# Kernel tuning notes

Measured on AMD Instinct MI355X. Metric: run time of the kernel, lower is better.

The kernel has to match this reference:

```python
import jax, jax.numpy as jnp
import numpy as np

DEPTH = 2
DIM = 512
FF = 2048
INNER = 32
VOCAB = 8192
B = 2
L = 512
LN_EPS = 1e-5


def _layer_norm(x, g, b):
    m = jnp.mean(x, axis=-1, keepdims=True)
    v = jnp.var(x, axis=-1, keepdims=True)
    return (x - m) * jax.lax.rsqrt(v + LN_EPS) * g + b


def _sioconv_layer(x, wa, wx, v_re, v_im, h0_re, h0_im, w_ol):
    # x: [B, L, DIM] float32
    Bb, Ll, _ = x.shape
    I = v_re.shape[0]
    # complex gate a with magnitude sigmoid(log|a|^2)
    af = (x @ wa.T).reshape(Bb, Ll, I, 2)
    a = jax.lax.complex(af[..., 0], af[..., 1])
    m = jnp.square(af[..., 0]) + jnp.square(af[..., 1])
    a = a * jax.lax.rsqrt(m) * jax.nn.sigmoid(jnp.log(m))  # [B,L,I] complex
    # complex input x with magnitude |x| (x * rsqrt(|x|^2) * |x|^2)
    xf = (x @ wx.T).reshape(Bb, Ll, I, 2)
    xc = jax.lax.complex(xf[..., 0], xf[..., 1])
    mx = jnp.square(xf[..., 0]) + jnp.square(xf[..., 1])
    xc = xc * jax.lax.rsqrt(mx) * mx  # [B,L,I] complex
    # cumulative log-decay products: the original's FFT conv of the upper-
    # triangular a_ln against an all-ones matrix is exactly a cumsum along j.
    a_ln = jnp.log(a)  # [B,L,I]
    ii = jnp.arange(Ll)[:, None]
    jj = jnp.arange(Ll)[None, :]
    tri = jnp.where((jj >= ii)[None, None, :, :],
                    jnp.transpose(a_ln, (0, 2, 1))[:, :, None, :],
                    jnp.zeros((), a_ln.dtype))  # [B,I,L,L]: tri[b,d,i,j]=a_ln[b,j,d] for j>=i
    s = jnp.cumsum(tri, axis=3)
    # c[b,d,i,j] = prod_{t=i..j} a[b,t,d] for j>=i; =1 at j=i-1; 0 below.
    c = jnp.where((jj >= ii - 1)[None, None, :, :], jnp.exp(s), jnp.zeros((), s.dtype))
    V = jax.lax.complex(v_re, v_im)
    Vinv = jnp.linalg.inv(V)
    h0 = jax.lax.complex(h0_re, h0_im)  # [I]
    xct = jnp.transpose(xc, (0, 2, 1))  # [B,I,L]
    x_roll = jnp.roll(xct, 1, axis=2).at[:, :, 0].set(h0[None, :])
    # original builds C[b,l,m,n,o] = V diag(c) V^-1 then einsum; contract lazily:
    y = jnp.einsum('ko,bol->bkl', Vinv, x_roll)  # eigenbasis inputs [B,I,L]
    t = jnp.einsum('bkij,bki->bjk', c, y)        # recurrence in eigenbasis [B,L,I]
    h = jnp.einsum('bjk,nk->bjn', t, V)          # back to state basis [B,L,I]
    h = h.at[:, -1, :].add(xc[:, -1, :])         # last step input (others already in c via j=i-1 band)
    return jnp.real(h) @ w_ol.T


def setup_inputs() -> dict:
    key = jax.random.key(0)
    ks = jax.random.split(key, 16)
    f = lambda k, shp: jax.random.normal(k, shp, dtype=jnp.float32)
    return {
        'x': f(ks[0], (B, L, VOCAB)),
        'w_in': f(ks[1], (DIM, VOCAB)) * VOCAB ** -0.5,
        'b_in': jnp.zeros((DIM,), jnp.float32),
        'ln1_g': jnp.ones((DEPTH, DIM), jnp.float32),
        'ln1_b': jnp.zeros((DEPTH, DIM), jnp.float32),
        'wa': f(ks[2], (DEPTH, 2 * INNER, DIM)) * DIM ** -0.5,
        'wx': f(ks[3], (DEPTH, 2 * INNER, DIM)) * DIM ** -0.5,
        'v_re': f(ks[4], (DEPTH, INNER, INNER)),
        'v_im': f(ks[5], (DEPTH, INNER, INNER)),
        'h0_re': f(ks[6], (DEPTH, INNER)),
        'h0_im': f(ks[7], (DEPTH, INNER)),
        'w_ol': f(ks[8], (DEPTH, DIM, INNER)) * INNER ** -0.5,
        'ln2_g': jnp.ones((DEPTH, DIM), jnp.float32),
        'ln2_b': jnp.zeros((DEPTH, DIM), jnp.float32),
        'w1': f(ks[9], (DEPTH, FF, DIM)) * DIM ** -0.5,
        'b1': jnp.zeros((DEPTH, FF), jnp.float32),
        'w2': f(ks[10], (DEPTH, DIM, FF)) * FF ** -0.5,
        'b2': jnp.zeros((DEPTH, DIM), jnp.float32),
        'lnl_g': jnp.ones((DIM,), jnp.float32),
        'lnl_b': jnp.zeros((DIM,), jnp.float32),
        'w_out': f(ks[11], (VOCAB, DIM)) * DIM ** -0.5,
        'b_out': jnp.zeros((VOCAB,), jnp.float32),
    }


def reference(x, w_in, b_in, ln1_g, ln1_b, wa, wx, v_re, v_im, h0_re, h0_im,
              w_ol, ln2_g, ln2_b, w1, b1, w2, b2, lnl_g, lnl_b, w_out, b_out):
    h = x @ w_in.T + b_in  # [B,L,DIM]
    for d in range(DEPTH):
        r = h
        z = _layer_norm(h, ln1_g[d], ln1_b[d])
        z = _sioconv_layer(z, wa[d], wx[d], v_re[d], v_im[d], h0_re[d], h0_im[d], w_ol[d])
        h = z + r
        r = h
        z = _layer_norm(h, ln2_g[d], ln2_b[d])
        z = jax.nn.silu(z @ w1[d].T + b1[d]) @ w2[d].T + b2[d]
        h = z + r
    h = _layer_norm(h, lnl_g, lnl_b)
    return h @ w_out.T + b_out
```

## Files before the change

### kernel.cpp

```cpp
#include <hip/hip_runtime.h>
#include <stdint.h>

#define DEPTHC 2
#define DIMC   512
#define FFC    2048
#define INNERC 32
#define VOCABC 8192
#define BC     2
#define LC     512
#define NTOK   1024

typedef _Float16 f16;
typedef __attribute__((ext_vector_type(8))) _Float16 f16x8;
typedef __attribute__((ext_vector_type(4))) float f32x4;

__device__ __forceinline__ float2 cmul2(float2 a, float2 b){
    return make_float2(a.x*b.x - a.y*b.y, a.x*b.y + a.y*b.x);
}
__device__ __forceinline__ float2 cadd2(float2 a, float2 b){
    return make_float2(a.x + b.x, a.y + b.y);
}

__device__ __forceinline__ void gl_lds16(const void* g, void* l){
    __builtin_amdgcn_global_load_lds(
        (const __attribute__((address_space(1))) unsigned int*)g,
        (__attribute__((address_space(3))) unsigned int*)l, 16, 0, 0);
}

__device__ __forceinline__ void cvt16(const float* s, f16* d){
    float4 v0 = ((const float4*)s)[0], v1 = ((const float4*)s)[1];
    float4 v2 = ((const float4*)s)[2], v3 = ((const float4*)s)[3];
    union { f16 h[16]; float4 f4[2]; } u;
    u.h[0]=(f16)v0.x; u.h[1]=(f16)v0.y; u.h[2]=(f16)v0.z; u.h[3]=(f16)v0.w;
    u.h[4]=(f16)v1.x; u.h[5]=(f16)v1.y; u.h[6]=(f16)v1.z; u.h[7]=(f16)v1.w;
    u.h[8]=(f16)v2.x; u.h[9]=(f16)v2.y; u.h[10]=(f16)v2.z; u.h[11]=(f16)v2.w;
    u.h[12]=(f16)v3.x; u.h[13]=(f16)v3.y; u.h[14]=(f16)v3.z; u.h[15]=(f16)v3.w;
    ((float4*)d)[0] = u.f4[0]; ((float4*)d)[1] = u.f4[1];
}

__global__ __launch_bounds__(256) void k_prep(
    const float* __restrict__ s1, const float* __restrict__ s2,
    const float* __restrict__ s3, const float* __restrict__ s4,
    const float* __restrict__ wa4, const float* __restrict__ wx4,
    f16* __restrict__ d1, f16* __restrict__ d2,
    f16* __restrict__ d3, f16* __restrict__ d4, f16* __restrict__ wgb,
    int n1, int n2, int n3, int n4,
    const float* __restrict__ v_re, const float* __restrict__ v_im,
    const float* __restrict__ h0re, const float* __restrict__ h0im,
    float2* __restrict__ vinv, float2* __restrict__ h0c)
{
    __shared__ float2 M[32][64];
    if (blockIdx.x < 2){
        const int d = blockIdx.x;
        const int tid = threadIdx.x;
        const int c = tid & 63;
        const int wv = tid >> 6;
        if (tid < 32) h0c[d*32 + tid] = make_float2(h0re[d*32 + tid], h0im[d*32 + tid]);
#pragma unroll
        for (int rr = 0; rr < 8; ++rr){
            int r = wv*8 + rr;
            float re, im;
            if (c < 32){ re = v_re[d*1024 + r*32 + c]; im = v_im[d*1024 + r*32 + c]; }
            else       { re = (c - 32 == r) ? 1.f : 0.f; im = 0.f; }
            M[r][c] = make_float2(re, im);
        }
        __syncthreads();
#pragma unroll 1
        for (int col = 0; col < 32; ++col){
            float2 prow = M[col][c];
            float pvx = __shfl(prow.x, col, 64);
            float pvy = __shfl(prow.y, col, 64);
            float dm = pvx*pvx + pvy*pvy;
            float ir = pvx/dm, ii = -pvy/dm;
            float2 nv = make_float2(prow.x*ir - prow.y*ii, prow.x*ii + prow.y*ir);
#pragma unroll
            for (int rr = 0; rr < 8; ++rr){
                int r = wv*8 + rr;
                if (r == col) continue;
                float2 f  = M[r][col];
                float2 m0 = M[r][c];
                m0.x -= f.x*nv.x - f.y*nv.y;
                m0.y -= f.x*nv.y + f.y*nv.x;
                M[r][c] = m0;
            }
            __syncthreads();
        }
        if (c >= 32){
#pragma unroll
            for (int rr = 0; rr < 8; ++rr){
                int r = wv*8 + rr;
                float2 dv = M[r][r];
                float dm = dv.x*dv.x + dv.y*dv.y;
                float ir = dv.x/dm, ii = -dv.y/dm;
                float2 m0 = M[r][c];
                vinv[d*1024 + r*32 + (c - 32)] =
                    make_float2(m0.x*ir - m0.y*ii, m0.x*ii + m0.y*ir);
            }
        }
        return;
    }
    long long i = ((long long)(blockIdx.x - 2) * 256 + threadIdx.x) * 16;
    const float* s; f16* d;
    if (i < n1){ s = s1; d = d1; }
    else { i -= n1;
        if (i < n2){ s = s2; d = d2; }
        else { i -= n2;
            if (i < n3){ s = s3; d = d3; }
            else { i -= n3;
                if (i < n4){ s = s4; d = d4; }
                else {
                    i -= n4;
                    if (i >= 131072) return;
                    const float* gs; f16* gd;
                    if (i < 65536){
                        int dd = (int)(i >> 15), rem = (int)(i & 32767);
                        gs = wa4 + i; gd = wgb + dd*65536 + rem;
                    } else {
                        long long e2 = i - 65536;
                        int dd = (int)(e2 >> 15), rem = (int)(e2 & 32767);
                        gs = wx4 + e2; gd = wgb + dd*65536 + 32768 + rem;
                    }
                    cvt16(gs, gd);
                    return;
                }
            }
        }
    }
    cvt16(s + i, d + i);
}

template<int MT, int NT, int MODE, int ASRC>
__global__ __launch_bounds__(256) void k_gemmT(
    const void* __restrict__ Av, const f16* __restrict__ Bw,
    void* __restrict__ C, const float* __restrict__ bias,
    int N, int K, int klen, int partStride,
    float2* __restrict__ a_tp, float2* __restrict__ xcp)
{
    constexpr int RM = MT/32, RN = NT/32;
    __shared__ __align__(16) f16 As[MT*64];
    __shared__ __align__(16) f16 Bs[NT*64];
    const int tid = threadIdx.x;
    const int m0 = blockIdx.y * MT;
    const int n0 = blockIdx.x * NT;
    const int kbeg = blockIdx.z * klen;
    const int l = tid & 63;
    const int w = tid >> 6;
    const int fr = l & 15;
    const int fq = l >> 4;
    const int kx = l & 7;
    const int wm = (w >> 1) * (MT/2);
    const int wn = (w & 1) * (NT/2);
    const int srow = tid >> 3;
    const int schunk = (tid & 7) ^ (srow & 7);
    const f16*   gA16 = (const f16*)Av + (ASRC ? 0 : ((size_t)(m0 + srow) * K + kbeg + schunk * 8));
    const float* gA32 = (const float*)Av + (ASRC ? ((size_t)(m0 + srow) * K + kbeg + (tid & 7) * 8) : 0);
    const f16* gB = Bw + (size_t)(n0 + srow) * K + kbeg + schunk * 8;
    const size_t rowskip = (size_t)32 * K;
    f16* lA = As + tid * 8;
    f16* lAw = As + srow * 64 + schunk * 8;
    f16* lB = Bs + tid * 8;
    f32x4 acc[RM][RN];
#pragma unroll
    for (int i = 0; i < RM; ++i)
#pragma unroll
        for (int j = 0; j < RN; ++j)
            acc[i][j] = (f32x4){0.f, 0.f, 0.f, 0.f};
    for (int kk = 0; kk < klen; kk += 64){
        __syncthreads();
        if (ASRC){
#pragma unroll
            for (int i = 0; i < MT/32; ++i){
                float4 va = *(const float4*)(gA32 + i*rowskip);
                float4 vb = *(const float4*)(gA32 + i*rowskip + 4);
                union { f16 h[8]; f16x8 v; } u;
                u.h[0]=(f16)va.x; u.h[1]=(f16)va.y; u.h[2]=(f16)va.z; u.h[3]=(f16)va.w;
                u.h[4]=(f16)vb.x; u.h[5]=(f16)vb.y; u.h[6]=(f16)vb.z; u.h[7]=(f16)vb.w;
                *(f16x8*)(lAw + i*2048) = u.v;
            }
            gA32 += 64;
        } else {
#pragma unroll
            for (int i = 0; i < MT/32; ++i) gl_lds16(gA16 + i*rowskip, lA + i*2048);
            gA16 += 64;
        }
#pragma unroll
        for (int i = 0; i < NT/32; ++i) gl_lds16(gB + i*rowskip, lB + i*2048);
        gB += 64;
        __syncthreads();
#pragma unroll
        for (int h = 0; h < 2; ++h){
            f16x8 af[RM], bf[RN];
#pragma unroll
            for (int i = 0; i < RM; ++i)
                af[i] = *(const f16x8*)(As + (wm + 16*i + fr) * 64 + (((h*4 + fq) ^ kx)) * 8);
#pragma unroll
            for (int j = 0; j < RN; ++j)
                bf[j] = *(const f16x8*)(Bs + (wn + 16*j + fr) * 64 + (((h*4 + fq) ^ kx)) * 8);
#pragma unroll
            for (int i = 0; i < RM; ++i)
#pragma unroll
                for (int j = 0; j < RN; ++j)
                    acc[i][j] = __builtin_amdgcn_mfma_f32_16x16x32_f16(af[i], bf[j], acc[i][j], 0, 0, 0);
        }
    }
#pragma unroll
    for (int i = 0; i < RM; ++i)
#pragma unroll
        for (int j = 0; j < RN; ++j)
#pragma unroll
            for (int r = 0; r < 4; ++r){
                int row = m0 + wm + 16*i + fq*4 + r;
                int col = n0 + wn + 16*j + fr;
                if (MODE == 1){
                    ((f16*)C + (size_t)blockIdx.z * partStride)[(size_t)row * N + col] = (f16)acc[i][j][r];
                } else if (MODE == 0){
                    ((float*)C)[(size_t)row * N + col] = acc[i][j][r] + bias[col];
                } else if (MODE == 2){
                    float v = acc[i][j][r] + bias[col];
                    ((f16*)C)[(size_t)row * N + col] = (f16)(v / (1.f + __expf(-v)));
                } else {
                    float val = acc[i][j][r];
                    float pv = __shfl_xor(val, 1, 64);
                    if (!(fr & 1)){
                        float re = val, im = pv;
                        int bb = row >> 9, t = row & 511;
                        float m2 = re*re + im*im;
                        if (col < 64){
                            int k = col >> 1;
                            float sa = rsqrtf(m2) * (m2 / (1.f + m2));
                            a_tp[(size_t)(bb*INNERC + k)*LC + t] = make_float2(re*sa, im*sa);
                        } else {
                            int k = (col - 64) >> 1;
                            float sx = sqrtf(m2);
                            xcp[(size_t)row*INNERC + k] = make_float2(re*sx, im*sx);
                        }
                    }
                }
            }
}

__global__ __launch_bounds__(128) void k_ln1(
    const f16* __restrict__ part, const float* __restrict__ bias,
    const float* __restrict__ res, const float* __restrict__ g,
    const float* __restrict__ b, f16* __restrict__ out,
    float* __restrict__ hout, int n)
{
    int row = blockIdx.x;
    int tid = threadIdx.x;
    __shared__ float sw[2], qw[2];
    float v[4]; float s = 0.f, q = 0.f;
#pragma unroll
    for (int j = 0; j < 4; ++j){
        int c = tid + 128*j;
        int idx = row*DIMC + c;
        float t = bias[c];
        if (res) t += res[idx];
#pragma unroll
        for (int z = 0; z < 8; ++z) t += (float)part[(size_t)z * n + idx];
        if (hout) hout[idx] = t;
        v[j] = t; s += t; q += t*t;
    }
    for (int off = 32; off; off >>= 1){ s += __shfl_down(s, off, 64); q += __shfl_down(q, off, 64); }
    if ((tid & 63) == 0){ sw[tid >> 6] = s; qw[tid >> 6] = q; }
    __syncthreads();
    float S = sw[0] + sw[1], Q = qw[0] + qw[1];
    float m = S / DIMC;
    float rstd = rsqrtf(Q / DIMC - m*m + 1e-5f);
#pragma unroll
    for (int j = 0; j < 4; ++j){
        int c = tid + 128*j;
        out[(size_t)row*DIMC + c] = (f16)((v[j] - m)*rstd*g[c] + b[c]);
    }
}

__global__ __launch_bounds__(64) void k_scan(
    const float2* __restrict__ a_t, const float2* __restrict__ xc,
    const float2* __restrict__ vinv, const float2* __restrict__ h0c,
    float2* __restrict__ e)
{
    int bk = blockIdx.x;
    int l = threadIdx.x;
    int bb = bk >> 5, k = bk & 31;
    float2 vrow[32];
#pragma unroll
    for (int o = 0; o < 32; ++o) vrow[o] = vinv[k*32 + o];
    int base = bk * LC + l * 8;
    float2 av[8], wv[8];
#pragma unroll
    for (int j = 0; j < 8; ++j) av[j] = a_t[base + j];
#pragma unroll
    for (int j = 0; j < 8; ++j){
        int t = l*8 + j;
        const float2* src = (t == 0) ? h0c : (xc + (size_t)(bb*LC + t - 1) * INNERC);
        float2 acc = make_float2(0.f, 0.f);
#pragma unroll
        for (int o = 0; o < 32; o += 2){
            float4 qq = *(const float4*)(src + o);
            acc.x += vrow[o].x*qq.x - vrow[o].y*qq.y;
            acc.y += vrow[o].x*qq.y + vrow[o].y*qq.x;
            acc.x += vrow[o+1].x*qq.z - vrow[o+1].y*qq.w;
            acc.y += vrow[o+1].x*qq.w + vrow[o+1].y*qq.z;
        }
        wv[j] = acc;
    }
    float2 A = make_float2(1.f, 0.f), Bc = make_float2(0.f, 0.f);
#pragma unroll
    for (int j = 0; j < 8; ++j){
        Bc = cmul2(av[j], cadd2(Bc, wv[j]));
        A  = cmul2(av[j], A);
    }
    for (int off = 1; off < 64; off <<= 1){
        float Apx = __shfl_up(A.x,  off, 64), Apy = __shfl_up(A.y,  off, 64);
        float Bpx = __shfl_up(Bc.x, off, 64), Bpy = __shfl_up(Bc.y, off, 64);
        if (l >= off){
            float2 Ap = make_float2(Apx, Apy), Bp = make_float2(Bpx, Bpy);
            Bc = cadd2(cmul2(A, Bp), Bc);
            A  = cmul2(A, Ap);
        }
    }
    float ex = __shfl_up(Bc.x, 1, 64), ey = __shfl_up(Bc.y, 1, 64);
    float2 ecur = (l == 0) ? make_float2(0.f, 0.f) : make_float2(ex, ey);
    size_t obase = ((size_t)bb*LC + l*8) * INNERC + k;
#pragma unroll
    for (int j = 0; j < 8; ++j){
        ecur = cmul2(av[j], cadd2(ecur, wv[j]));
        e[obase + (size_t)j * INNERC] = ecur;
    }
}

__global__ __launch_bounds__(128) void k_siout_ln(
    const float2* __restrict__ e, const float2* __restrict__ xc,
    const float* __restrict__ vre, const float* __restrict__ vim,
    const float* __restrict__ wol, const float* __restrict__ res,
    const float* __restrict__ g2, const float* __restrict__ b2,
    float* __restrict__ hout, f16* __restrict__ zout)
{
    int bt = blockIdx.x;
    int tid = threadIdx.x;
    __shared__ float hr[INNERC];
    __shared__ float2 er[INNERC];
    __shared__ float sw[2], qw[2];
    if (tid < 32) er[tid] = e[(size_t)bt*INNERC + tid];
    __syncthreads();
    if (tid < 32){
        const float* vrr = vre + tid*INNERC;
        const float* vir = vim + tid*INNERC;
        float acc = xc[(size_t)bt*INNERC + tid].x;
#pragma unroll
        for (int k2 = 0; k2 < 32; ++k2) acc += vrr[k2]*er[k2].x - vir[k2]*er[k2].y;
        hr[tid] = acc;
    }
    __syncthreads();
    float v[4]; float s = 0.f, q = 0.f;
#pragma unroll
    for (int j = 0; j < 4; ++j){
        int n = tid + 128*j;
        float val = res[(size_t)bt*DIMC + n];
        const float* wr = wol + (size_t)n * INNERC;
#pragma unroll
        for (int i = 0; i < 32; ++i) val += hr[i]*wr[i];
        hout[(size_t)bt*DIMC + n] = val;
        v[j] = val; s += val; q += val*val;
    }
    for (int off = 32; off; off >>= 1){ s += __shfl_down(s, off, 64); q += __shfl_down(q, off, 64); }
    if ((tid & 63) == 0){ sw[tid >> 6] = s; qw[tid >> 6] = q; }
    __syncthreads();
    float S = sw[0] + sw[1], Q = qw[0] + qw[1];
    float m = S / DIMC;
    float rstd = rsqrtf(Q / DIMC - m*m + 1e-5f);
#pragma unroll
    for (int j = 0; j < 4; ++j){
        int n = tid + 128*j;
        zout[(size_t)bt*DIMC + n] = (f16)((v[j] - m)*rstd*g2[n] + b2[n]);
    }
}

extern "C" void kernel_launch(void* const* d_in, const int* in_sizes, int n_in,
                              void* d_out, int out_size, void* d_ws, size_t ws_size,
                              hipStream_t stream)
{
    const float* x     = (const float*)d_in[0];
    const float* w_in  = (const float*)d_in[1];
    const float* b_in  = (const float*)d_in[2];
    const float* ln1_g = (const float*)d_in[3];
    const float* ln1_b = (const float*)d_in[4];
    const float* wa    = (const float*)d_in[5];
    const float* wx    = (const float*)d_in[6];
    const float* v_re  = (const float*)d_in[7];
    const float* v_im  = (const float*)d_in[8];
    const float* h0_re = (const float*)d_in[9];
    const float* h0_im = (const float*)d_in[10];
    const float* w_ol  = (const float*)d_in[11];
    const float* ln2_g = (const float*)d_in[12];
    const float* ln2_b = (const float*)d_in[13];
    const float* w1    = (const float*)d_in[14];
    const float* b1    = (const float*)d_in[15];
    const float* w2    = (const float*)d_in[16];
    const float* b2    = (const float*)d_in[17];
    const float* lnl_g = (const float*)d_in[18];
    const float* lnl_b = (const float*)d_in[19];
    const float* w_out = (const float*)d_in[20];
    const float* b_out = (const float*)d_in[21];

    char* p = (char*)d_ws;
    f16* wib  = (f16*)p;   p += (size_t)DIMC * VOCABC * 2;
    f16* wob  = (f16*)p;   p += (size_t)VOCABC * DIMC * 2;
    f16* w1b  = (f16*)p;   p += (size_t)DEPTHC * FFC * DIMC * 2;
    f16* w2b  = (f16*)p;   p += (size_t)DEPTHC * DIMC * FFC * 2;
    f16* wgb  = (f16*)p;   p += (size_t)DEPTHC * 2*INNERC*2 * DIMC * 2;
    float* h1 = (float*)p; p += (size_t)NTOK * DIMC * 4;
    float* h2 = (float*)p; p += (size_t)NTOK * DIMC * 4;
    float* h3 = (float*)p; p += (size_t)NTOK * DIMC * 4;
    f16* zb   = (f16*)p;   p += (size_t)NTOK * DIMC * 2;
    f16* ffb  = (f16*)p;   p += (size_t)NTOK * FFC * 2;
    f16* pbuf = (f16*)p;   p += (size_t)8 * NTOK * DIMC * 2;
    float2* a_t = (float2*)p; p += (size_t)BC * INNERC * LC * 8;
    float2* xc  = (float2*)p; p += (size_t)NTOK * INNERC * 8;
    float2* ev  = (float2*)p; p += (size_t)NTOK * INNERC * 8;
    float2* vinv = (float2*)p; p += (size_t)DEPTHC * INNERC * INNERC * 8;
    float2* h0c  = (float2*)p; p += (size_t)DEPTHC * INNERC * 8;

    {
        const int n1 = DIMC*VOCABC, n2 = DEPTHC*FFC*DIMC,
                  n3 = DEPTHC*DIMC*FFC, n4 = VOCABC*DIMC;
        int blocks = (n1 + n2 + n3 + n4 + 131072) / 4096 + 2;
        k_prep<<<blocks, 256, 0, stream>>>(w_in, w1, w2, w_out, wa, wx,
                                           wib, w1b, w2b, wob, wgb,
                                           n1, n2, n3, n4,
                                           v_re, v_im, h0_re, h0_im, vinv, h0c);
    }

    {
        dim3 g(DIMC/128, NTOK/64, 8);
        k_gemmT<64,128,1,1><<<g, 256, 0, stream>>>(x, wib, pbuf, nullptr, DIMC, VOCABC, VOCABC/8, NTOK*DIMC,
                                                   nullptr, nullptr);
    }

    for (int d = 0; d < DEPTHC; ++d){
        float* cur = (d == 0) ? h1 : h3;
        float* hb  = h2;
        const float* redBias = (d == 0) ? b_in : (b2 + (d-1)*DIMC);
        const float* redRes  = (d == 0) ? nullptr : h2;
        k_ln1<<<NTOK, 128, 0, stream>>>(pbuf, redBias, redRes,
                                        ln1_g + d*DIMC, ln1_b + d*DIMC, zb, cur, NTOK*DIMC);
        {
            dim3 g(1, NTOK/32, 1);
            k_gemmT<32,128,3,0><<<g, 256, 0, stream>>>(zb, wgb + (size_t)d*128*DIMC, nullptr, nullptr,
                                                       128, DIMC, DIMC, 0, a_t, xc);
        }
        k_scan<<<BC*INNERC, 64, 0, stream>>>(a_t, xc, vinv + d*INNERC*INNERC, h0c + d*INNERC, ev);
        k_siout_ln<<<NTOK, 128, 0, stream>>>(ev, xc, v_re + d*INNERC*INNERC, v_im + d*INNERC*INNERC,
                                             w_ol + (size_t)d*DIMC*INNERC, cur,
                                             ln2_g + d*DIMC, ln2_b + d*DIMC, hb, zb);
        {
            dim3 g(FFC/128, NTOK/64, 1);
            k_gemmT<64,128,2,0><<<g, 256, 0, stream>>>(zb, w1b + (size_t)d*FFC*DIMC, ffb, b1 + d*FFC,
                                                       FFC, DIMC, DIMC, 0, nullptr, nullptr);
        }
        {
            dim3 g(DIMC/128, NTOK/64, 8);
            k_gemmT<64,128,1,0><<<g, 256, 0, stream>>>(ffb, w2b + (size_t)d*DIMC*FFC, pbuf, nullptr,
                                                       DIMC, FFC, FFC/8, NTOK*DIMC, nullptr, nullptr);
        }
    }
    k_ln1<<<NTOK, 128, 0, stream>>>(pbuf, b2 + (DEPTHC-1)*DIMC, h2, lnl_g, lnl_b, zb, nullptr, NTOK*DIMC);
    {
        dim3 g(VOCABC/128, NTOK/128, 1);
        k_gemmT<128,128,0,0><<<g, 256, 0, stream>>>(zb, wob, (float*)d_out, b_out, VOCABC, DIMC, DIMC, 0,
                                                    nullptr, nullptr);
    }
    (void)in_sizes; (void)n_in; (void)out_size; (void)ws_size;
}
```

Baseline: 342.2 us.

## Pre-convert input activations to fp16 in prep and invert V in registers

Adds the 1024x8192 input x to the bulk fp32-to-fp16 conversion in the prep kernel, so the input GEMM reads fp16 A tiles (ASRC=0) instead of converting fp32 on the fly. It also rewrites the 32x32 complex Gauss-Jordan inversion to keep each column in registers of a single wave and use shuffles, removing LDS traffic and per-step block barriers. The price is an extra 16 MB fp16 workspace write plus a reread of x, and heavier register use in the inversion wave.

New measurement: 373.1 us. 9.0% more time.

```diff
diff --git a/kernel.cpp b/kernel.cpp
--- a/kernel.cpp
+++ b/kernel.cpp
@@ -39,89 +39,79 @@
 }
 
 __global__ __launch_bounds__(256) void k_prep(
-    const float* __restrict__ s1, const float* __restrict__ s2,
-    const float* __restrict__ s3, const float* __restrict__ s4,
+    const float* __restrict__ s0, const float* __restrict__ s1,
+    const float* __restrict__ s2, const float* __restrict__ s3,
+    const float* __restrict__ s4,
     const float* __restrict__ wa4, const float* __restrict__ wx4,
-    f16* __restrict__ d1, f16* __restrict__ d2,
+    f16* __restrict__ d0, f16* __restrict__ d1, f16* __restrict__ d2,
     f16* __restrict__ d3, f16* __restrict__ d4, f16* __restrict__ wgb,
-    int n1, int n2, int n3, int n4,
+    int n0, int n1, int n2, int n3, int n4,
     const float* __restrict__ v_re, const float* __restrict__ v_im,
     const float* __restrict__ h0re, const float* __restrict__ h0im,
     float2* __restrict__ vinv, float2* __restrict__ h0c)
 {
-    __shared__ float2 M[32][64];
     if (blockIdx.x < 2){
         const int d = blockIdx.x;
         const int tid = threadIdx.x;
-        const int c = tid & 63;
-        const int wv = tid >> 6;
-        if (tid < 32) h0c[d*32 + tid] = make_float2(h0re[d*32 + tid], h0im[d*32 + tid]);
-#pragma unroll
-        for (int rr = 0; rr < 8; ++rr){
-            int r = wv*8 + rr;
-            float re, im;
-            if (c < 32){ re = v_re[d*1024 + r*32 + c]; im = v_im[d*1024 + r*32 + c]; }
-            else       { re = (c - 32 == r) ? 1.f : 0.f; im = 0.f; }
-            M[r][c] = make_float2(re, im);
-        }
-        __syncthreads();
-#pragma unroll 1
-        for (int col = 0; col < 32; ++col){
-            float2 prow = M[col][c];
-            float pvx = __shfl(prow.x, col, 64);
-            float pvy = __shfl(prow.y, col, 64);
-            float dm = pvx*pvx + pvy*pvy;
-            float ir = pvx/dm, ii = -pvy/dm;
-            float2 nv = make_float2(prow.x*ir - prow.y*ii, prow.x*ii + prow.y*ir);
-#pragma unroll
-            for (int rr = 0; rr < 8; ++rr){
-                int r = wv*8 + rr;
-                if (r == col) continue;
-                float2 f  = M[r][col];
-                float2 m0 = M[r][c];
-                m0.x -= f.x*nv.x - f.y*nv.y;
-                m0.y -= f.x*nv.y + f.y*nv.x;
-                M[r][c] = m0;
+        if (tid >= 64) return;
+        const int c = tid;
+        if (c < 32) h0c[d*32 + c] = make_float2(h0re[d*32 + c], h0im[d*32 + c]);
+        float2 col[32];
+#pragma unroll
+        for (int r = 0; r < 32; ++r){
+            if (c < 32) col[r] = make_float2(v_re[d*1024 + r*32 + c], v_im[d*1024 + r*32 + c]);
+            else        col[r] = make_float2((c - 32) == r ? 1.f : 0.f, 0.f);
+        }
+#pragma unroll
+        for (int k = 0; k < 32; ++k){
+            float px = __shfl(col[k].x, k, 64);
+            float py = __shfl(col[k].y, k, 64);
+            float dm = px*px + py*py;
+            float ir = px/dm, ii = -py/dm;
+            float2 nv = make_float2(col[k].x*ir - col[k].y*ii, col[k].x*ii + col[k].y*ir);
+            col[k] = nv;
+#pragma unroll
+            for (int r = 0; r < 32; ++r){
+                if (r == k) continue;
+                float fx = __shfl(col[r].x, k, 64);
+                float fy = __shfl(col[r].y, k, 64);
+                col[r].x -= fx*nv.x - fy*nv.y;
+                col[r].y -= fx*nv.y + fy*nv.x;
             }
-            __syncthreads();
         }
         if (c >= 32){
 #pragma unroll
-            for (int rr = 0; rr < 8; ++rr){
-                int r = wv*8 + rr;
-                float2 dv = M[r][r];
-                float dm = dv.x*dv.x + dv.y*dv.y;
-                float ir = dv.x/dm, ii = -dv.y/dm;
-                float2 m0 = M[r][c];
-                vinv[d*1024 + r*32 + (c - 32)] =
-                    make_float2(m0.x*ir - m0.y*ii, m0.x*ii + m0.y*ir);
-            }
+            for (int r = 0; r < 32; ++r)
+                vinv[d*1024 + r*32 + (c - 32)] = col[r];
         }
         return;
     }
     long long i = ((long long)(blockIdx.x - 2) * 256 + threadIdx.x) * 16;
     const float* s; f16* d;
-    if (i < n1){ s = s1; d = d1; }
-    else { i -= n1;
-        if (i < n2){ s = s2; d = d2; }
-        else { i -= n2;
-            if (i < n3){ s = s3; d = d3; }
-            else { i -= n3;
-                if (i < n4){ s = s4; d = d4; }
-                else {
-                    i -= n4;
-                    if (i >= 131072) return;
-                    const float* gs; f16* gd;
-                    if (i < 65536){
-                        int dd = (int)(i >> 15), rem = (int)(i & 32767);
-                        gs = wa4 + i; gd = wgb + dd*65536 + rem;
-                    } else {
-                        long long e2 = i - 65536;
-                        int dd = (int)(e2 >> 15), rem = (int)(e2 & 32767);
-                        gs = wx4 + e2; gd = wgb + dd*65536 + 32768 + rem;
+    if (i < n0){ s = s0; d = d0; }
+    else { i -= n0;
+        if (i < n1){ s = s1; d = d1; }
+        else { i -= n1;
+            if (i < n2){ s = s2; d = d2; }
+            else { i -= n2;
+                if (i < n3){ s = s3; d = d3; }
+                else { i -= n3;
+                    if (i < n4){ s = s4; d = d4; }
+                    else {
+                        i -= n4;
+                        if (i >= 131072) return;
+                        const float* gs; f16* gd;
+                        if (i < 65536){
+                            int dd = (int)(i >> 15), rem = (int)(i & 32767);
+                            gs = wa4 + i; gd = wgb + dd*65536 + rem;
+                        } else {
+                            long long e2 = i - 65536;
+                            int dd = (int)(e2 >> 15), rem = (int)(e2 & 32767);
+                            gs = wx4 + e2; gd = wgb + dd*65536 + 32768 + rem;
+                        }
+                        cvt16(gs, gd);
+                        return;
                     }
-                    cvt16(gs, gd);
-                    return;
                 }
             }
         }
@@ -403,6 +393,7 @@
     const float* b_out = (const float*)d_in[21];
 
     char* p = (char*)d_ws;
+    f16* xb   = (f16*)p;   p += (size_t)NTOK * VOCABC * 2;
     f16* wib  = (f16*)p;   p += (size_t)DIMC * VOCABC * 2;
     f16* wob  = (f16*)p;   p += (size_t)VOCABC * DIMC * 2;
     f16* w1b  = (f16*)p;   p += (size_t)DEPTHC * FFC * DIMC * 2;
@@ -421,18 +412,18 @@
     float2* h0c  = (float2*)p; p += (size_t)DEPTHC * INNERC * 8;
 
     {
-        const int n1 = DIMC*VOCABC, n2 = DEPTHC*FFC*DIMC,
+        const int n0 = NTOK*VOCABC, n1 = DIMC*VOCABC, n2 = DEPTHC*FFC*DIMC,
                   n3 = DEPTHC*DIMC*FFC, n4 = VOCABC*DIMC;
-        int blocks = (n1 + n2 + n3 + n4 + 131072) / 4096 + 2;
-        k_prep<<<blocks, 256, 0, stream>>>(w_in, w1, w2, w_out, wa, wx,
-                                           wib, w1b, w2b, wob, wgb,
-                                           n1, n2, n3, n4,
+        int blocks = (n0 + n1 + n2 + n3 + n4 + 131072) / 4096 + 2;
+        k_prep<<<blocks, 256, 0, stream>>>(x, w_in, w1, w2, w_out, wa, wx,
+                                           xb, wib, w1b, w2b, wob, wgb,
+                                           n0, n1, n2, n3, n4,
                                            v_re, v_im, h0_re, h0_im, vinv, h0c);
     }
 
     {
         dim3 g(DIMC/128, NTOK/64, 8);
-        k_gemmT<64,128,1,1><<<g, 256, 0, stream>>>(x, wib, pbuf, nullptr, DIMC, VOCABC, VOCABC/8, NTOK*DIMC,
+        k_gemmT<64,128,1,0><<<g, 256, 0, stream>>>(xb, wib, pbuf, nullptr, DIMC, VOCABC, VOCABC/8, NTOK*DIMC,
                                                    nullptr, nullptr);
     }
 
```
